# Performance work log

Hardware: AMD Instinct MI355X
Metric: run time of the kernel (lower is better)

Reference implementation:

```python
import jax, jax.numpy as jnp
import numpy as np

N, F, C, H = 6144, 128, 64, 4
NEG = -1.0e10


def setup_inputs() -> dict:
    key = jax.random.key(0)
    ks = jax.random.split(key, 8)
    X = jax.random.normal(ks[0], (N, F), dtype=jnp.float32)
    A = (jax.random.uniform(ks[1], (N, N)) < 0.01).astype(jnp.float32)  # sparse-ish 0/1 adjacency
    A = A.at[jnp.arange(N), jnp.arange(N)].set(1.0)  # self loops so every row has a neighbor
    s = 1.0 / np.sqrt(F)
    W1 = jax.random.normal(ks[2], (H, F, C), dtype=jnp.float32) * s
    W2 = jax.random.normal(ks[3], (H, F, C), dtype=jnp.float32) * s
    a_self = jax.random.normal(ks[4], (H, C), dtype=jnp.float32) * (1.0 / np.sqrt(C))
    a_neigh = jax.random.normal(ks[5], (H, C), dtype=jnp.float32) * (1.0 / np.sqrt(C))
    bias = jnp.zeros((H, C), dtype=jnp.float32)
    return {"X": X, "A": A, "W1": W1, "W2": W2, "a_self": a_self, "a_neigh": a_neigh, "bias": bias}


def reference(X, A, W1, W2, a_self, a_neigh, bias):
    # Per-head projections: [H, N, C]
    feats = jnp.einsum('nf,hfc->hnc', X, W1)
    feats2 = jnp.einsum('nf,hfc->hnc', X, W2)
    # Attention logits: self term + transposed neighbor term -> [H, N, N]
    att_s = jnp.einsum('hnc,hc->hn', feats, a_self)
    att_n = jnp.einsum('hnc,hc->hn', feats, a_neigh)
    dense = att_s[:, :, None] + att_n[:, None, :]
    dense = jnp.where(dense > 0, dense, 0.2 * dense)  # LeakyReLU(0.2)
    dense = dense + NEG * (1.0 - A)[None, :, :]       # additive adjacency mask
    attn = jax.nn.softmax(dense, axis=-1)
    # Dropout layers are identity at inference.
    node = jnp.einsum('hnm,hmc->hnc', attn, feats) + feats2 + bias[:, None, :]
    out = jnp.mean(node, axis=0)  # attn_heads_reduction='average'
    return jax.nn.relu(out)
```

## Files before the change

kernel.cpp:

```cpp
#include <hip/hip_runtime.h>
#include <hip/hip_bf16.h>


#define N_NODES 6144
#define F_DIM   128
#define C_DIM   64
#define H_HEADS 4
#define HC      (H_HEADS * C_DIM)
#define MAXKW   128

typedef unsigned short u16;
typedef float v4f __attribute__((ext_vector_type(4)));

__global__ __launch_bounds__(256) void proj_kernel(
    const float* __restrict__ X,
    const float* __restrict__ W1, const float* __restrict__ W2,
    const float* __restrict__ a_self, const float* __restrict__ a_neigh,
    u16* __restrict__ featsB, float* __restrict__ feats2T,
    float* __restrict__ attsT, float* __restrict__ attnT)
{
    const int rt    = blockIdx.x;
    const int z     = blockIdx.y;
    const int h     = z >> 1;
    const int which = z & 1;

    const float* W = (which ? W2 : W1) + h * F_DIM * C_DIM;

    __shared__ float  Xs[64][132];
    __shared__ float4 Ws4[128][17];

    const int tid = threadIdx.x;

    {
        const float4* Xg = (const float4*)(X + (size_t)rt * 64 * F_DIM);
        for (int u = tid; u < 64 * 32; u += 256) {
            const int r = u >> 5, q = u & 31;
            *(float4*)&Xs[r][4 * q] = Xg[u];
        }
        const float4* Wg = (const float4*)W;
        for (int u = tid; u < 128 * 16; u += 256) {
            Ws4[u >> 4][u & 15] = Wg[u];
        }
    }
    __syncthreads();

    const int tx = tid & 15;
    const int ty = tid >> 4;

    float acc[4][4] = {};
    for (int k = 0; k < 128; k += 4) {
        const float4 b0 = Ws4[k + 0][tx];
        const float4 b1 = Ws4[k + 1][tx];
        const float4 b2 = Ws4[k + 2][tx];
        const float4 b3 = Ws4[k + 3][tx];
        #pragma unroll
        for (int i = 0; i < 4; ++i) {
            const float4 x = *(const float4*)&Xs[4 * ty + i][k];
            acc[i][0] += x.x * b0.x + x.y * b1.x + x.z * b2.x + x.w * b3.x;
            acc[i][1] += x.x * b0.y + x.y * b1.y + x.z * b2.y + x.w * b3.y;
            acc[i][2] += x.x * b0.z + x.y * b1.z + x.z * b2.z + x.w * b3.z;
            acc[i][3] += x.x * b0.w + x.y * b1.w + x.z * b2.w + x.w * b3.w;
        }
    }

    __syncthreads();
    float* Ct = &Xs[0][0];

    #pragma unroll
    for (int i = 0; i < 4; ++i) {
        const int r    = 4 * ty + i;
        const int node = rt * 64 + r;
        if (which == 0) {
            u16 p0 = __bfloat16_as_ushort(__float2bfloat16(acc[i][0]));
            u16 p1 = __bfloat16_as_ushort(__float2bfloat16(acc[i][1]));
            u16 p2 = __bfloat16_as_ushort(__float2bfloat16(acc[i][2]));
            u16 p3 = __bfloat16_as_ushort(__float2bfloat16(acc[i][3]));
            ushort4 pk; pk.x = p0; pk.y = p1; pk.z = p2; pk.w = p3;
            *(ushort4*)&featsB[(size_t)node * HC + h * C_DIM + 4 * tx] = pk;
            Ct[r * 65 + 4 * tx + 0] = acc[i][0];
            Ct[r * 65 + 4 * tx + 1] = acc[i][1];
            Ct[r * 65 + 4 * tx + 2] = acc[i][2];
            Ct[r * 65 + 4 * tx + 3] = acc[i][3];
        } else {
            *(float4*)&feats2T[(size_t)node * HC + h * C_DIM + 4 * tx] =
                make_float4(acc[i][0], acc[i][1], acc[i][2], acc[i][3]);
        }
    }

    if (which == 0) {
        __syncthreads();
        if (tid < 64) {
            const float* as_ = a_self  + h * C_DIM;
            const float* an_ = a_neigh + h * C_DIM;
            float s = 0.f, n = 0.f;
            #pragma unroll 8
            for (int c = 0; c < C_DIM; ++c) {
                const float v = Ct[tid * 65 + c];
                s += v * as_[c];
                n += v * an_[c];
            }
            const int node = rt * 64 + tid;
            attsT[node * H_HEADS + h] = s;
            attnT[node * H_HEADS + h] = n;
        }
    }
}

__global__ __launch_bounds__(256) void agg_kernel(
    const float* __restrict__ A,
    const u16* __restrict__ featsB, const float* __restrict__ feats2T,
    const float* __restrict__ attsT, const float* __restrict__ attnT,
    const float* __restrict__ bias,
    float* __restrict__ out)
{
    const int w    = threadIdx.x >> 6;
    const int lane = threadIdx.x & 63;
    const int i    = blockIdx.x * 4 + w;

    __shared__ int idxs[4][MAXKW];
    int* idx_w = idxs[w];

    const unsigned long long ltmask = (1ull << lane) - 1ull;
    const v4f* Arow = (const v4f*)(A + (size_t)i * N_NODES);

    const int    hsel = lane >> 4;
    const float  si   = attsT[4 * i + hsel];
    const float* anp  = attnT + hsel;
    const uint2* fb   = (const uint2*)featsB;

    float a0 = 0.f, a1 = 0.f, a2 = 0.f, a3 = 0.f;
    float z  = 0.f;
    int   base = 0;

    #define UPFMA(q, e)                                                     \
        {                                                                   \
            a0 += (e) * __uint_as_float((q).x << 16);                       \
            a1 += (e) * __uint_as_float((q).x & 0xffff0000u);               \
            a2 += (e) * __uint_as_float((q).y << 16);                       \
            a3 += (e) * __uint_as_float((q).y & 0xffff0000u);               \
        }
    #define EXPW(an, e)                                                     \
        float e;                                                            \
        {                                                                   \
            float l = si + (an);                                            \
            l = (l > 0.f) ? l : 0.2f * l;                                   \
            e = __expf(l);                                                  \
        }

    v4f cur[6];
    #pragma unroll
    for (int g = 0; g < 6; ++g)
        cur[g] = __builtin_nontemporal_load(Arow + lane + 64 * g);

    #pragma unroll
    for (int ch = 0; ch < 4; ++ch) {
        v4f nxt[6];
        if (ch < 3) {
            #pragma unroll
            for (int g = 0; g < 6; ++g)
                nxt[g] = __builtin_nontemporal_load(Arow + lane + 64 * ((ch + 1) * 6 + g));
        }

        const int start = (base < MAXKW) ? base : MAXKW;
        #pragma unroll
        for (int g = 0; g < 6; ++g) {
            const int col = 4 * (lane + 64 * (ch * 6 + g));
            #pragma unroll
            for (int m = 0; m < 4; ++m) {
                const float x = (m == 0) ? cur[g].x : (m == 1) ? cur[g].y
                              : (m == 2) ? cur[g].z : cur[g].w;
                const bool p = (x > 0.5f);
                const unsigned long long mask = __ballot(p);
                if (p) {
                    const int pos = base + (int)__popcll(mask & ltmask);
                    if (pos < MAXKW) idx_w[pos] = col + m;
                }
                base += (int)__popcll(mask);
            }
        }
        const int end = (base < MAXKW) ? base : MAXKW;

        int k = start;
        for (; k + 4 <= end; k += 4) {
            const int j0 = idx_w[k + 0];
            const int j1 = idx_w[k + 1];
            const int j2 = idx_w[k + 2];
            const int j3 = idx_w[k + 3];
            const float an0 = anp[4 * (size_t)j0];
            const float an1 = anp[4 * (size_t)j1];
            const float an2 = anp[4 * (size_t)j2];
            const float an3 = anp[4 * (size_t)j3];
            const uint2 q0 = fb[(size_t)j0 * 64 + lane];
            const uint2 q1 = fb[(size_t)j1 * 64 + lane];
            const uint2 q2 = fb[(size_t)j2 * 64 + lane];
            const uint2 q3 = fb[(size_t)j3 * 64 + lane];
            EXPW(an0, e0) EXPW(an1, e1) EXPW(an2, e2) EXPW(an3, e3)
            z += e0 + e1 + e2 + e3;
            UPFMA(q0, e0) UPFMA(q1, e1) UPFMA(q2, e2) UPFMA(q3, e3)
        }
        for (; k < end; ++k) {
            const int   j  = idx_w[k];
            const float an = anp[4 * (size_t)j];
            const uint2 q  = fb[(size_t)j * 64 + lane];
            EXPW(an, e)
            z += e;
            UPFMA(q, e)
        }

        if (ch < 3) {
            #pragma unroll
            for (int g = 0; g < 6; ++g) cur[g] = nxt[g];
        }
    }
    #undef UPFMA
    #undef EXPW

    const float zinv = 1.0f / z;
    const float4 f2 = *(const float4*)&feats2T[(size_t)i * HC + 4 * lane];
    const float4 b4 = *(const float4*)&bias[4 * lane];
    float s0 = a0 * zinv + f2.x + b4.x;
    float s1 = a1 * zinv + f2.y + b4.y;
    float s2 = a2 * zinv + f2.z + b4.z;
    float s3 = a3 * zinv + f2.w + b4.w;
    s0 += __shfl_xor(s0, 16); s0 += __shfl_xor(s0, 32);
    s1 += __shfl_xor(s1, 16); s1 += __shfl_xor(s1, 32);
    s2 += __shfl_xor(s2, 16); s2 += __shfl_xor(s2, 32);
    s3 += __shfl_xor(s3, 16); s3 += __shfl_xor(s3, 32);
    if (lane < 16) {
        float4 o;
        o.x = fmaxf(0.25f * s0, 0.f);
        o.y = fmaxf(0.25f * s1, 0.f);
        o.z = fmaxf(0.25f * s2, 0.f);
        o.w = fmaxf(0.25f * s3, 0.f);
        *(float4*)&out[(size_t)i * C_DIM + 4 * lane] = o;
    }
}

extern "C" void kernel_launch(void* const* d_in, const int* in_sizes, int n_in,
                              void* d_out, int out_size, void* d_ws, size_t ws_size,
                              hipStream_t stream) {
    const float* X       = (const float*)d_in[0];
    const float* A       = (const float*)d_in[1];
    const float* W1      = (const float*)d_in[2];
    const float* W2      = (const float*)d_in[3];
    const float* a_self  = (const float*)d_in[4];
    const float* a_neigh = (const float*)d_in[5];
    const float* bias    = (const float*)d_in[6];
    float* out = (float*)d_out;

    float* ws      = (float*)d_ws;
    float* feats2T = ws;
    float* attsT   = feats2T + (size_t)N_NODES * HC;
    float* attnT   = attsT   + (size_t)N_NODES * H_HEADS;
    u16*   featsB  = (u16*)(attnT + (size_t)N_NODES * H_HEADS);

    dim3 grid1(N_NODES / 64, H_HEADS * 2);
    proj_kernel<<<grid1, 256, 0, stream>>>(X, W1, W2, a_self, a_neigh,
                                           featsB, feats2T, attsT, attnT);

    agg_kernel<<<N_NODES / 4, 256, 0, stream>>>(A, featsB, feats2T, attsT, attnT, bias, out);
}
```

Measured before the change: 249.9 us.

## Scan full adjacency row before gathering, unroll gather loop by eight

The per-chunk interleaving of adjacency scanning and neighbor gathering, which prefetched the next chunk of A while processing the current one, is removed. The kernel now scans the whole A row first to build the neighbor index list, then runs one gather/accumulate loop over all neighbors. That loop is unrolled by eight and reads indices from shared memory with vector loads. The aim is more memory-level parallelism in the gather and less loop overhead, at the cost of losing the overlap between streaming A and the gather work.

```diff
diff --git a/kernel.cpp b/kernel.cpp
--- a/kernel.cpp
+++ b/kernel.cpp
@@ -120,55 +120,22 @@
     __shared__ int idxs[4][MAXKW];
     int* idx_w = idxs[w];
 
+    const v4f* Arow = (const v4f*)(A + (size_t)i * N_NODES);
     const unsigned long long ltmask = (1ull << lane) - 1ull;
-    const v4f* Arow = (const v4f*)(A + (size_t)i * N_NODES);
-
-    const int    hsel = lane >> 4;
-    const float  si   = attsT[4 * i + hsel];
-    const float* anp  = attnT + hsel;
-    const uint2* fb   = (const uint2*)featsB;
-
-    float a0 = 0.f, a1 = 0.f, a2 = 0.f, a3 = 0.f;
-    float z  = 0.f;
-    int   base = 0;
-
-    #define UPFMA(q, e)                                                     \
-        {                                                                   \
-            a0 += (e) * __uint_as_float((q).x << 16);                       \
-            a1 += (e) * __uint_as_float((q).x & 0xffff0000u);               \
-            a2 += (e) * __uint_as_float((q).y << 16);                       \
-            a3 += (e) * __uint_as_float((q).y & 0xffff0000u);               \
-        }
-    #define EXPW(an, e)                                                     \
-        float e;                                                            \
-        {                                                                   \
-            float l = si + (an);                                            \
-            l = (l > 0.f) ? l : 0.2f * l;                                   \
-            e = __expf(l);                                                  \
-        }
-
-    v4f cur[6];
-    #pragma unroll
-    for (int g = 0; g < 6; ++g)
-        cur[g] = __builtin_nontemporal_load(Arow + lane + 64 * g);
-
+    int base = 0;
     #pragma unroll
     for (int ch = 0; ch < 4; ++ch) {
-        v4f nxt[6];
-        if (ch < 3) {
-            #pragma unroll
-            for (int g = 0; g < 6; ++g)
-                nxt[g] = __builtin_nontemporal_load(Arow + lane + 64 * ((ch + 1) * 6 + g));
-        }
-
-        const int start = (base < MAXKW) ? base : MAXKW;
+        v4f v[6];
+        #pragma unroll
+        for (int g = 0; g < 6; ++g)
+            v[g] = __builtin_nontemporal_load(Arow + lane + 64 * (ch * 6 + g));
         #pragma unroll
         for (int g = 0; g < 6; ++g) {
             const int col = 4 * (lane + 64 * (ch * 6 + g));
             #pragma unroll
             for (int m = 0; m < 4; ++m) {
-                const float x = (m == 0) ? cur[g].x : (m == 1) ? cur[g].y
-                              : (m == 2) ? cur[g].z : cur[g].w;
+                const float x = (m == 0) ? v[g].x : (m == 1) ? v[g].y
+                              : (m == 2) ? v[g].z : v[g].w;
                 const bool p = (x > 0.5f);
                 const unsigned long long mask = __ballot(p);
                 if (p) {
@@ -178,39 +145,65 @@
                 base += (int)__popcll(mask);
             }
         }
-        const int end = (base < MAXKW) ? base : MAXKW;
-
-        int k = start;
-        for (; k + 4 <= end; k += 4) {
-            const int j0 = idx_w[k + 0];
-            const int j1 = idx_w[k + 1];
-            const int j2 = idx_w[k + 2];
-            const int j3 = idx_w[k + 3];
-            const float an0 = anp[4 * (size_t)j0];
-            const float an1 = anp[4 * (size_t)j1];
-            const float an2 = anp[4 * (size_t)j2];
-            const float an3 = anp[4 * (size_t)j3];
-            const uint2 q0 = fb[(size_t)j0 * 64 + lane];
-            const uint2 q1 = fb[(size_t)j1 * 64 + lane];
-            const uint2 q2 = fb[(size_t)j2 * 64 + lane];
-            const uint2 q3 = fb[(size_t)j3 * 64 + lane];
-            EXPW(an0, e0) EXPW(an1, e1) EXPW(an2, e2) EXPW(an3, e3)
-            z += e0 + e1 + e2 + e3;
-            UPFMA(q0, e0) UPFMA(q1, e1) UPFMA(q2, e2) UPFMA(q3, e3)
-        }
-        for (; k < end; ++k) {
-            const int   j  = idx_w[k];
-            const float an = anp[4 * (size_t)j];
-            const uint2 q  = fb[(size_t)j * 64 + lane];
-            EXPW(an, e)
-            z += e;
-            UPFMA(q, e)
-        }
-
-        if (ch < 3) {
-            #pragma unroll
-            for (int g = 0; g < 6; ++g) cur[g] = nxt[g];
-        }
+    }
+    const int K = min(base, MAXKW);
+
+    const int    hsel = lane >> 4;
+    const float  si   = attsT[4 * i + hsel];
+    const float* anp  = attnT + hsel;
+    const uint2* fb   = (const uint2*)featsB;
+
+    float a0 = 0.f, a1 = 0.f, a2 = 0.f, a3 = 0.f;
+    float z  = 0.f;
+
+    #define UPFMA(q, e)                                                     \
+        {                                                                   \
+            a0 += (e) * __uint_as_float((q).x << 16);                       \
+            a1 += (e) * __uint_as_float((q).x & 0xffff0000u);               \
+            a2 += (e) * __uint_as_float((q).y << 16);                       \
+            a3 += (e) * __uint_as_float((q).y & 0xffff0000u);               \
+        }
+    #define EXPW(an, e)                                                     \
+        float e;                                                            \
+        {                                                                   \
+            float l = si + (an);                                            \
+            l = (l > 0.f) ? l : 0.2f * l;                                   \
+            e = __expf(l);                                                  \
+        }
+
+    int k = 0;
+    for (; k + 8 <= K; k += 8) {
+        const int4 j0 = *(const int4*)&idx_w[k];
+        const int4 j1 = *(const int4*)&idx_w[k + 4];
+        const float an0 = anp[4 * (size_t)j0.x];
+        const float an1 = anp[4 * (size_t)j0.y];
+        const float an2 = anp[4 * (size_t)j0.z];
+        const float an3 = anp[4 * (size_t)j0.w];
+        const float an4 = anp[4 * (size_t)j1.x];
+        const float an5 = anp[4 * (size_t)j1.y];
+        const float an6 = anp[4 * (size_t)j1.z];
+        const float an7 = anp[4 * (size_t)j1.w];
+        const uint2 q0 = fb[(size_t)j0.x * 64 + lane];
+        const uint2 q1 = fb[(size_t)j0.y * 64 + lane];
+        const uint2 q2 = fb[(size_t)j0.z * 64 + lane];
+        const uint2 q3 = fb[(size_t)j0.w * 64 + lane];
+        const uint2 q4 = fb[(size_t)j1.x * 64 + lane];
+        const uint2 q5 = fb[(size_t)j1.y * 64 + lane];
+        const uint2 q6 = fb[(size_t)j1.z * 64 + lane];
+        const uint2 q7 = fb[(size_t)j1.w * 64 + lane];
+        EXPW(an0, e0) EXPW(an1, e1) EXPW(an2, e2) EXPW(an3, e3)
+        EXPW(an4, e4) EXPW(an5, e5) EXPW(an6, e6) EXPW(an7, e7)
+        z += (e0 + e1 + e2 + e3) + (e4 + e5 + e6 + e7);
+        UPFMA(q0, e0) UPFMA(q1, e1) UPFMA(q2, e2) UPFMA(q3, e3)
+        UPFMA(q4, e4) UPFMA(q5, e5) UPFMA(q6, e6) UPFMA(q7, e7)
+    }
+    for (; k < K; ++k) {
+        const int   j  = idx_w[k];
+        const float an = anp[4 * (size_t)j];
+        const uint2 q  = fb[(size_t)j * 64 + lane];
+        EXPW(an, e)
+        z += e;
+        UPFMA(q, e)
     }
     #undef UPFMA
     #undef EXPW
```

Result: no change. 246.9 us (-1.2%).
